# Optimization experiments

Hardware: AMD Instinct MI355X
Metric: run time of the kernel (lower is better)

The kernel has to match this reference:

```python
import jax
import jax.numpy as jnp
from jax import lax
import numpy as np

D_MODEL = 768
D_INNER = 1536  # d_model * expand_factor
D_STATE = 16
D_CONV = 4
BATCH = 2
SEQ = 2048
EPS = 1e-5


def silu(x):
    return x * jax.nn.sigmoid(x)


def setup_inputs() -> dict:
    key = jax.random.key(0)
    ks = jax.random.split(key, 24)
    n = lambda k, shape, s=0.1: jax.random.normal(k, shape, dtype=jnp.float32) * s
    inp = {
        "x": jax.random.normal(ks[0], (BATCH, SEQ, D_MODEL), dtype=jnp.float32),
        "ln_g": jnp.ones((D_MODEL,), jnp.float32),
        "ln_b": jnp.zeros((D_MODEL,), jnp.float32),
        "W_in": n(ks[1], (D_INNER, D_MODEL)),
        "b_in": n(ks[2], (D_INNER,)),
        "conv_w": n(ks[3], (D_INNER, 1, D_CONV), 0.02),
        "conv_b": jnp.zeros((D_INNER,), jnp.float32),
        "W_A": n(ks[4], (D_STATE, D_INNER)),
        "b_A": n(ks[5], (D_STATE,)),
        "W_B": n(ks[6], (D_STATE, D_INNER)),
        "b_B": n(ks[7], (D_STATE,)),
        "W_C": n(ks[8], (D_STATE, D_INNER)),
        "b_C": n(ks[9], (D_STATE,)),
        "W_dt": n(ks[10], (D_STATE, D_INNER)),
        "b_dt": n(ks[11], (D_STATE,)),
        "W_S": n(ks[12], (2 * D_INNER, D_INNER)),
        "b_S": n(ks[13], (2 * D_INNER,)),
        "W_gate": n(ks[14], (D_INNER, D_MODEL)),
        "b_gate": n(ks[15], (D_INNER,)),
        "W_out": n(ks[16], (D_MODEL, D_INNER)),
        "b_out": n(ks[17], (D_MODEL,)),
    }
    return inp


def reference(x, ln_g, ln_b, W_in, b_in, conv_w, conv_b, W_A, b_A, W_B, b_B,
              W_C, b_C, W_dt, b_dt, W_S, b_S, W_gate, b_gate, W_out, b_out):
    residual = x
    # LayerNorm
    mu = jnp.mean(x, axis=-1, keepdims=True)
    var = jnp.mean((x - mu) ** 2, axis=-1, keepdims=True)
    xn = (x - mu) * lax.rsqrt(var + EPS) * ln_g + ln_b
    # in projection -> [B, S, D_INNER]
    xp = xn @ W_in.T + b_in
    # depthwise causal conv1d over time
    k = conv_w.shape[-1]
    xc = jnp.moveaxis(xp, 1, 2)  # [B, D, L]
    xc = lax.conv_general_dilated(
        xc, conv_w, window_strides=(1,), padding=[(k - 1, 0)],
        dimension_numbers=("NCH", "OIH", "NCH"),
        feature_group_count=xc.shape[1])
    xc = xc + conv_b[None, :, None]
    xa = silu(jnp.moveaxis(xc, 1, 2))  # [B, S, D]
    # selective gating of SSM input (S_b computed but unused, as in source)
    S = xa @ W_S.T + b_S
    d = xa.shape[-1]
    S_a = jax.nn.sigmoid(S[..., :d])
    u = xa * S_a  # [B, S, D]
    # input-dependent SSM params [B, S, N]
    A = -jnp.exp(u @ W_A.T + b_A)
    dt = jnp.exp(u @ W_dt.T + b_dt)
    Bm = u @ W_B.T + b_B
    Cm = u @ W_C.T + b_C
    decay = jnp.exp(A * dt)  # [B, S, N]

    def step(h, inputs):
        dec_t, B_t, C_t, u_t = inputs  # [B,N],[B,N],[B,N],[B,D]
        h = h * dec_t[:, None, :] + B_t[:, None, :] * u_t[:, :, None]  # [B,D,N]
        y = jnp.einsum("bdn,bn->bd", h, C_t)
        return h, y

    h0 = jnp.zeros((u.shape[0], u.shape[2], decay.shape[-1]), u.dtype)
    scan_in = (jnp.moveaxis(decay, 1, 0), jnp.moveaxis(Bm, 1, 0),
               jnp.moveaxis(Cm, 1, 0), jnp.moveaxis(u, 1, 0))
    _, ys = lax.scan(step, h0, scan_in)
    y = jnp.moveaxis(ys, 0, 1)  # [B, S, D]
    # output gating + projection + residual
    gate = silu(xn @ W_gate.T + b_gate)
    out = (gate * y) @ W_out.T + b_out + residual
    return out
```

## Files before the change

### kernel.cpp

```cpp
#include <hip/hip_runtime.h>


typedef unsigned short u16;
using short8 = __attribute__((ext_vector_type(8))) short;
using f32x4  = __attribute__((ext_vector_type(4))) float;

#define BATCH 2
#define SEQ   2048
#define DM    768
#define DI    1536
#define NIG   (2*DI)
#define NST   16
#define LCH   64
#define NCH   32
#define NTOK  (BATCH*SEQ)

__device__ __forceinline__ u16 f2b(float x) {
  unsigned u = __float_as_uint(x);
  u += 0x7FFFu + ((u >> 16) & 1u);
  return (u16)(u >> 16);
}
__device__ __forceinline__ float b2f(u16 v) { return __uint_as_float((unsigned)v << 16); }
__device__ __forceinline__ float sigmoidf_(float x) { return 1.f / (1.f + expf(-x)); }
__device__ __forceinline__ float siluf_(float x) { return x / (1.f + expf(-x)); }

#define N_IG   (NIG * DM / 4)
#define N_WS   (DI * DI / 4)
#define N_WO   (DM * DI / 4)
#define N_WAB  (64 * DI / 4)
#define N_CAST (N_IG + N_WS + N_WO + N_WAB + NIG + 64)

__global__ __launch_bounds__(256) void cast_all(
    const float* __restrict__ Wi, const float* __restrict__ Wg,
    const float* __restrict__ bi, const float* __restrict__ bg,
    const float* __restrict__ WS, const float* __restrict__ WO,
    const float* __restrict__ WA, const float* __restrict__ Wdt,
    const float* __restrict__ WB, const float* __restrict__ WC,
    const float* __restrict__ bA, const float* __restrict__ bdt,
    const float* __restrict__ bB, const float* __restrict__ bC,
    u16* __restrict__ Wigb, float* __restrict__ biasig,
    u16* __restrict__ WSb, u16* __restrict__ Woutb,
    u16* __restrict__ Wabcd, float* __restrict__ bias64) {
  int i = blockIdx.x * 256 + threadIdx.x;
  if (i < N_IG) {
    int i4 = i * 4, r = i4 / DM, c = i4 % DM;
    const float* src = (r < DI) ? Wi + (size_t)r * DM + c : Wg + (size_t)(r - DI) * DM + c;
    float4 v = *(const float4*)src;
    ushort4 o; o.x = f2b(v.x); o.y = f2b(v.y); o.z = f2b(v.z); o.w = f2b(v.w);
    ((ushort4*)Wigb)[i] = o;
  } else if (i < N_IG + N_WS) {
    int j = i - N_IG;
    float4 v = ((const float4*)WS)[j];
    ushort4 o; o.x = f2b(v.x); o.y = f2b(v.y); o.z = f2b(v.z); o.w = f2b(v.w);
    ((ushort4*)WSb)[j] = o;
  } else if (i < N_IG + N_WS + N_WO) {
    int j = i - N_IG - N_WS;
    float4 v = ((const float4*)WO)[j];
    ushort4 o; o.x = f2b(v.x); o.y = f2b(v.y); o.z = f2b(v.z); o.w = f2b(v.w);
    ((ushort4*)Woutb)[j] = o;
  } else if (i < N_IG + N_WS + N_WO + N_WAB) {
    int j = i - N_IG - N_WS - N_WO;
    int i4 = j * 4, r = i4 / DI, c = i4 % DI;
    const float* src = (r < 16) ? WA + (size_t)r * DI
                     : (r < 32) ? Wdt + (size_t)(r - 16) * DI
                     : (r < 48) ? WB + (size_t)(r - 32) * DI
                                : WC + (size_t)(r - 48) * DI;
    float4 v = *(const float4*)(src + c);
    ushort4 o; o.x = f2b(v.x); o.y = f2b(v.y); o.z = f2b(v.z); o.w = f2b(v.w);
    ((ushort4*)Wabcd)[j] = o;
  } else if (i < N_IG + N_WS + N_WO + N_WAB + NIG) {
    int j = i - N_IG - N_WS - N_WO - N_WAB;
    biasig[j] = (j < DI) ? bi[j] : bg[j - DI];
  } else if (i < N_CAST) {
    int j = i - N_IG - N_WS - N_WO - N_WAB - NIG;
    bias64[j] = (j < 16) ? bA[j] : (j < 32) ? bdt[j - 16] : (j < 48) ? bB[j - 32] : bC[j - 48];
  }
}

__global__ __launch_bounds__(256) void ln_kernel(const float* __restrict__ x, const float* __restrict__ g,
                                                 const float* __restrict__ bb, u16* __restrict__ xn) {
  int m = blockIdx.x, tid = threadIdx.x;
  const float* xr = x + (size_t)m * DM;
  float v0 = xr[tid], v1 = xr[tid + 256], v2 = xr[tid + 512];
  float s  = v0 + v1 + v2;
  float s2 = fmaf(v0, v0, fmaf(v1, v1, v2 * v2));
  #pragma unroll
  for (int off = 32; off > 0; off >>= 1) { s += __shfl_down(s, off); s2 += __shfl_down(s2, off); }
  __shared__ float sh[8];
  int wave = tid >> 6, lane = tid & 63;
  if (lane == 0) { sh[wave] = s; sh[4 + wave] = s2; }
  __syncthreads();
  float S1 = sh[0] + sh[1] + sh[2] + sh[3];
  float S2 = sh[4] + sh[5] + sh[6] + sh[7];
  float mu = S1 * (1.f / DM);
  float var = S2 * (1.f / DM) - mu * mu;
  float rs = rsqrtf(var + 1e-5f);
  u16* o = xn + (size_t)m * DM;
  o[tid]       = f2b((v0 - mu) * rs * g[tid]       + bb[tid]);
  o[tid + 256] = f2b((v1 - mu) * rs * g[tid + 256] + bb[tid + 256]);
  o[tid + 512] = f2b((v2 - mu) * rs * g[tid + 512] + bb[tid + 512]);
}

__device__ __forceinline__ void gll16(const void* g, void* l) {
  __builtin_amdgcn_global_load_lds((const __attribute__((address_space(1))) void*)g,
                                   (__attribute__((address_space(3))) void*)l, 16, 0, 0);
}

template <int MODE, int BM>
__global__ __launch_bounds__(BM == 128 ? 512 : 256) void gemm_bt(
    const u16* __restrict__ A, const u16* __restrict__ B,
    const float* __restrict__ bias, const float* __restrict__ aux,
    const u16* __restrict__ auxb,
    float* __restrict__ C, u16* __restrict__ Cb,
    int M, int N, int K) {
  __shared__ __align__(16) u16 As[3][BM * 32];
  __shared__ __align__(16) u16 Bs[3][128 * 32];
  const int tid = threadIdx.x, wave = tid >> 6, lane = tid & 63;

  const int nbx = gridDim.x, nwg = nbx * gridDim.y;
  const int orig = blockIdx.y * nbx + blockIdx.x;
  const int cpx = nwg >> 3;
  const int swz = (orig & 7) * cpx + (orig >> 3);
  const int m0 = (swz / nbx) * BM, n0 = (swz % nbx) * 128;

  const int wm = (wave >> 1) * 32, wn = (wave & 1) * 64;
  const int fr = lane & 15, fq = lane >> 4;
  f32x4 acc[2][4] = {};

  const int c0 = tid;
  const u16* Ag0 = A + (size_t)(m0 + (c0 >> 2)) * K + ((c0 & 3) ^ ((c0 >> 3) & 3)) * 8;
  const u16* Bg0 = B + (size_t)(n0 + (c0 >> 2)) * K + ((c0 & 3) ^ ((c0 >> 3) & 3)) * 8;
  const int lofs = (wave * 64) * 8;
  const int c1 = tid + 256;
  const u16* Bg1 = B + (size_t)(n0 + (c1 >> 2)) * K + ((c1 & 3) ^ ((c1 >> 3) & 3)) * 8;
  const int lofs1 = (256 + wave * 64) * 8;

  int offA[2], offB[4];
  #pragma unroll
  for (int i = 0; i < 2; ++i) {
    int ra = wm + i * 16 + fr;
    offA[i] = ra * 32 + (fq ^ ((ra >> 1) & 3)) * 8;
  }
  #pragma unroll
  for (int i = 0; i < 4; ++i) {
    int rb = wn + i * 16 + fr;
    offB[i] = rb * 32 + (fq ^ ((rb >> 1) & 3)) * 8;
  }

  const int nk = K >> 5;

#define STAGE_BT(tt) { const int bb_ = (tt) % 3; \
                       gll16(Ag0 + (tt) * 32, (u16*)As[bb_] + lofs); \
                       gll16(Bg0 + (tt) * 32, (u16*)Bs[bb_] + lofs); \
                       if (BM == 64) gll16(Bg1 + (tt) * 32, (u16*)Bs[bb_] + lofs1); }
#define COMPUTE_BT(tt) { const u16* as_ = As[(tt) % 3]; const u16* bs_ = Bs[(tt) % 3]; \
    short8 av[2], bv[4]; \
    _Pragma("unroll") for (int i = 0; i < 2; ++i) av[i] = *(const short8*)(as_ + offA[i]); \
    _Pragma("unroll") for (int i = 0; i < 4; ++i) bv[i] = *(const short8*)(bs_ + offB[i]); \
    __builtin_amdgcn_s_setprio(1); \
    _Pragma("unroll") for (int mi = 0; mi < 2; ++mi) \
      _Pragma("unroll") for (int ni = 0; ni < 4; ++ni) \
        acc[mi][ni] = __builtin_amdgcn_mfma_f32_16x16x32_bf16(av[mi], bv[ni], acc[mi][ni], 0, 0, 0); \
    __builtin_amdgcn_s_setprio(0); }
#define WAIT1S() { if (BM == 128) asm volatile("s_waitcnt vmcnt(2)" ::: "memory"); \
                   else           asm volatile("s_waitcnt vmcnt(3)" ::: "memory"); }

  STAGE_BT(0); STAGE_BT(1);

  for (int t = 0; t < nk - 2; ++t) {
    WAIT1S();
    __builtin_amdgcn_s_barrier();
    STAGE_BT(t + 2);
    COMPUTE_BT(t);
  }
  WAIT1S();
  __builtin_amdgcn_s_barrier();
  COMPUTE_BT(nk - 2);
  asm volatile("s_waitcnt vmcnt(0)" ::: "memory");
  __builtin_amdgcn_s_barrier();
  COMPUTE_BT(nk - 1);
#undef STAGE_BT
#undef COMPUTE_BT
#undef WAIT1S

  #pragma unroll
  for (int ni = 0; ni < 4; ++ni) {
    int col = n0 + wn + ni * 16 + fr;
    float bv_ = bias[col];
    #pragma unroll
    for (int mi = 0; mi < 2; ++mi) {
      int row = m0 + wm + mi * 16 + fq * 4;
      #pragma unroll
      for (int j = 0; j < 4; ++j) {
        size_t off = (size_t)(row + j) * N + col;
        float z = acc[mi][ni][j] + bv_;
        if (MODE == 0) {
          C[off] = z + aux[off];
        } else if (MODE == 1) {
          Cb[off] = f2b(b2f(auxb[off]) * sigmoidf_(z));
        } else {
          Cb[off] = f2b(z);
        }
      }
    }
  }
}

__global__ __launch_bounds__(256) void gemm_abcd(const u16* __restrict__ A, const u16* __restrict__ B,
                                                 float* __restrict__ Zp, int M, int K) {
  __shared__ __align__(16) u16 As[2][64 * 64];
  __shared__ __align__(16) u16 Bs[2][64 * 64];
  const int tid = threadIdx.x, wave = tid >> 6, lane = tid & 63;
  const int m0 = blockIdx.x * 64;
  const int ks = blockIdx.y;
  const int Kq = K >> 2;
  const int kbase = ks * Kq;
  const int wm = wave * 16;
  const int fr = lane & 15, fq = lane >> 4;
  f32x4 acc[4] = {};

  const int c0 = tid, c1 = tid + 256;
  const u16* Ag0 = A + (size_t)(m0 + (c0 >> 3)) * K + kbase + ((c0 & 7) ^ ((c0 >> 3) & 7)) * 8;
  const u16* Ag1 = A + (size_t)(m0 + (c1 >> 3)) * K + kbase + ((c1 & 7) ^ ((c1 >> 3) & 7)) * 8;
  const u16* Bg0 = B + (size_t)(c0 >> 3) * K + kbase + ((c0 & 7) ^ ((c0 >> 3) & 7)) * 8;
  const u16* Bg1 = B + (size_t)(c1 >> 3) * K + kbase + ((c1 & 7) ^ ((c1 >> 3) & 7)) * 8;
  const int lo0 = (wave * 64) * 8;
  const int lo1 = (256 + wave * 64) * 8;

  int offAv[2], offBv[2][4];
  {
    int r = wm + fr;
    #pragma unroll
    for (int kk = 0; kk < 2; ++kk) offAv[kk] = r * 64 + ((kk * 4 + fq) ^ (r & 7)) * 8;
    #pragma unroll
    for (int i = 0; i < 4; ++i) {
      int rb = i * 16 + fr;
      #pragma unroll
      for (int kk = 0; kk < 2; ++kk) offBv[kk][i] = rb * 64 + ((kk * 4 + fq) ^ (rb & 7)) * 8;
    }
  }

  const int nk = Kq >> 6;
  gll16(Ag0, (u16*)As[0] + lo0);
  gll16(Ag1, (u16*)As[0] + lo1);
  gll16(Bg0, (u16*)Bs[0] + lo0);
  gll16(Bg1, (u16*)Bs[0] + lo1);

  for (int t = 0; t < nk; ++t) {
    __syncthreads();
    if (t + 1 < nk) {
      int ko = (t + 1) * 64;
      gll16(Ag0 + ko, (u16*)As[(t + 1) & 1] + lo0);
      gll16(Ag1 + ko, (u16*)As[(t + 1) & 1] + lo1);
      gll16(Bg0 + ko, (u16*)Bs[(t + 1) & 1] + lo0);
      gll16(Bg1 + ko, (u16*)Bs[(t + 1) & 1] + lo1);
    }
    const u16* as = As[t & 1];
    const u16* bs = Bs[t & 1];
    #pragma unroll
    for (int kk = 0; kk < 2; ++kk) {
      short8 av = *(const short8*)(as + offAv[kk]);
      short8 bv[4];
      #pragma unroll
      for (int i = 0; i < 4; ++i) bv[i] = *(const short8*)(bs + offBv[kk][i]);
      #pragma unroll
      for (int ni = 0; ni < 4; ++ni)
        acc[ni] = __builtin_amdgcn_mfma_f32_16x16x32_bf16(av, bv[ni], acc[ni], 0, 0, 0);
    }
  }

  float* zp = Zp + (size_t)ks * M * 64;
  #pragma unroll
  for (int ni = 0; ni < 4; ++ni) {
    int col = ni * 16 + fr;
    #pragma unroll
    for (int j = 0; j < 4; ++j) {
      int row = m0 + wm + fq * 4 + j;
      zp[(size_t)row * 64 + col] = acc[ni][j];
    }
  }
}

__global__ __launch_bounds__(256) void abcd_combine(const float* __restrict__ Zp, const float* __restrict__ bias64,
                                                    float* __restrict__ dec, float* __restrict__ Bm,
                                                    float* __restrict__ Cm, int M) {
  int idx = blockIdx.x * 256 + threadIdx.x;
  int row = idx >> 4, n = idx & 15;
  float zA = bias64[n], zDt = bias64[16 + n], zB = bias64[32 + n], zC = bias64[48 + n];
  #pragma unroll
  for (int ks = 0; ks < 4; ++ks) {
    const float* zp = Zp + ((size_t)ks * M + row) * 64;
    zA += zp[n]; zDt += zp[16 + n]; zB += zp[32 + n]; zC += zp[48 + n];
  }
  size_t o = (size_t)row * NST + n;
  dec[o] = expf(-expf(zA + zDt));
  Bm[o] = zB;
  Cm[o] = zC;
}

__global__ __launch_bounds__(256) void conv_silu(const u16* __restrict__ xpg, const float* __restrict__ cw,
                                                 const float* __restrict__ cb, u16* __restrict__ xab) {
  int idx = blockIdx.x * 256 + threadIdx.x;
  int d8 = idx % (DI / 8);
  int token = idx / (DI / 8);
  int t = token % SEQ;
  int d0 = d8 * 8;
  const short8* xv = (const short8*)(xpg + (size_t)token * NIG + d0);
  short8 z8 = {0, 0, 0, 0, 0, 0, 0, 0};
  short8 x3 = (t >= 3) ? xv[-3 * (NIG / 8)] : z8;
  short8 x2 = (t >= 2) ? xv[-2 * (NIG / 8)] : z8;
  short8 x1 = (t >= 1) ? xv[-1 * (NIG / 8)] : z8;
  short8 x0 = xv[0];
  const float4* cw4 = (const float4*)cw;
  float4 cbl = ((const float4*)cb)[d8 * 2], cbh = ((const float4*)cb)[d8 * 2 + 1];
  float cbv[8] = {cbl.x, cbl.y, cbl.z, cbl.w, cbh.x, cbh.y, cbh.z, cbh.w};
  short8 o;
  #pragma unroll
  for (int j = 0; j < 8; ++j) {
    float4 w = cw4[d0 + j];
    float a = cbv[j];
    a = fmaf(b2f((u16)x3[j]), w.x, a);
    a = fmaf(b2f((u16)x2[j]), w.y, a);
    a = fmaf(b2f((u16)x1[j]), w.z, a);
    a = fmaf(b2f((u16)x0[j]), w.w, a);
    o[j] = (short)f2b(siluf_(a));
  }
  *(short8*)(xab + (size_t)token * DI + d0) = o;
}

__global__ __launch_bounds__(256) void scan_phase1(const u16* __restrict__ ub, const float* __restrict__ dec,
                                                   const float* __restrict__ Bm, u16* __restrict__ lend,
                                                   float* __restrict__ P) {
  __shared__ __align__(16) float dl[LCH * NST], bl[LCH * NST];
  int bid = blockIdx.x;
  int dblk = bid % 6, b = (bid / 6) % BATCH, c = bid / (6 * BATCH);
  int d = dblk * 256 + threadIdx.x;
  int t0 = c * LCH;
  size_t base16 = (size_t)(b * SEQ + t0) * NST;
  for (int i = threadIdx.x; i < LCH * NST / 4; i += 256) {
    ((float4*)dl)[i] = ((const float4*)(dec + base16))[i];
    ((float4*)bl)[i] = ((const float4*)(Bm + base16))[i];
  }
  __syncthreads();
  float h[NST];
  #pragma unroll
  for (int n = 0; n < NST; ++n) h[n] = 0.f;
  const u16* up = ub + (size_t)(b * SEQ + t0) * DI + d;
  for (int t = 0; t < LCH; ++t) {
    float uu = b2f(up[(size_t)t * DI]);
    const f32x4* d4 = (const f32x4*)(dl + t * NST);
    const f32x4* b4 = (const f32x4*)(bl + t * NST);
    #pragma unroll
    for (int q = 0; q < 4; ++q) {
      f32x4 dd = d4[q], bb = b4[q];
      #pragma unroll
      for (int j = 0; j < 4; ++j) h[q * 4 + j] = fmaf(h[q * 4 + j], dd[j], bb[j] * uu);
    }
  }
  u16* lo = lend + ((size_t)(c * BATCH + b) * DI + d) * NST;
  short8 s0, s1;
  #pragma unroll
  for (int n = 0; n < 8; ++n) { s0[n] = (short)f2b(h[n]); s1[n] = (short)f2b(h[8 + n]); }
  ((short8*)lo)[0] = s0;
  ((short8*)lo)[1] = s1;
  if (dblk == 0 && threadIdx.x < NST) {
    float pr = 1.f;
    for (int t = 0; t < LCH; ++t) pr *= dl[t * NST + threadIdx.x];
    P[(size_t)(c * BATCH + b) * NST + threadIdx.x] = pr;
  }
}

__global__ __launch_bounds__(256) void scan_phase2(const u16* __restrict__ lend, const float* __restrict__ P,
                                                   u16* __restrict__ Hin) {
  int flat = blockIdx.x * 256 + threadIdx.x;
  int n = flat & 15;
  int d = (flat >> 4) % DI;
  int b = flat / (DI * NST);
  float h = 0.f;
  for (int c = 0; c < NCH; ++c) {
    size_t idx = ((size_t)(c * BATCH + b) * DI + d) * NST + n;
    Hin[idx] = f2b(h);
    h = fmaf(P[(size_t)(c * BATCH + b) * NST + n], h, b2f(lend[idx]));
  }
}

__global__ __launch_bounds__(256) void scan_phase3(const u16* __restrict__ ub, const float* __restrict__ dec,
                                                   const float* __restrict__ Bm, const float* __restrict__ Cm,
                                                   const u16* __restrict__ Hin, const u16* __restrict__ xpg,
                                                   u16* __restrict__ gy) {
  __shared__ __align__(16) float dl[LCH * NST], bl[LCH * NST], cl[LCH * NST];
  int bid = blockIdx.x;
  int dblk = bid % 6, b = (bid / 6) % BATCH, c = bid / (6 * BATCH);
  int d = dblk * 256 + threadIdx.x;
  int t0 = c * LCH;
  size_t base16 = (size_t)(b * SEQ + t0) * NST;
  for (int i = threadIdx.x; i < LCH * NST / 4; i += 256) {
    ((float4*)dl)[i] = ((const float4*)(dec + base16))[i];
    ((float4*)bl)[i] = ((const float4*)(Bm + base16))[i];
    ((float4*)cl)[i] = ((const float4*)(Cm + base16))[i];
  }
  __syncthreads();
  float h[NST];
  const short8* hi = (const short8*)(Hin + ((size_t)(c * BATCH + b) * DI + d) * NST);
  short8 h0 = hi[0], h1 = hi[1];
  #pragma unroll
  for (int n = 0; n < 8; ++n) { h[n] = b2f((u16)h0[n]); h[8 + n] = b2f((u16)h1[n]); }
  const u16* up = ub + (size_t)(b * SEQ + t0) * DI + d;
  const u16* gp = xpg + (size_t)(b * SEQ + t0) * NIG + DI + d;
  u16* yp = gy + (size_t)(b * SEQ + t0) * DI + d;
  for (int t = 0; t < LCH; ++t) {
    float uu = b2f(up[(size_t)t * DI]);
    const f32x4* d4 = (const f32x4*)(dl + t * NST);
    const f32x4* b4 = (const f32x4*)(bl + t * NST);
    const f32x4* c4 = (const f32x4*)(cl + t * NST);
    float acc = 0.f;
    #pragma unroll
    for (int q = 0; q < 4; ++q) {
      f32x4 dd = d4[q], bb = b4[q], cc = c4[q];
      #pragma unroll
      for (int j = 0; j < 4; ++j) {
        h[q * 4 + j] = fmaf(h[q * 4 + j], dd[j], bb[j] * uu);
        acc = fmaf(h[q * 4 + j], cc[j], acc);
      }
    }
    float g = b2f(gp[(size_t)t * NIG]);
    yp[(size_t)t * DI] = f2b(siluf_(g) * acc);
  }
}

extern "C" void kernel_launch(void* const* d_in, const int* in_sizes, int n_in,
                              void* d_out, int out_size, void* d_ws, size_t ws_size,
                              hipStream_t stream) {
  const float* x      = (const float*)d_in[0];
  const float* ln_g   = (const float*)d_in[1];
  const float* ln_b   = (const float*)d_in[2];
  const float* W_in   = (const float*)d_in[3];
  const float* b_in   = (const float*)d_in[4];
  const float* conv_w = (const float*)d_in[5];
  const float* conv_b = (const float*)d_in[6];
  const float* W_A    = (const float*)d_in[7];
  const float* b_A    = (const float*)d_in[8];
  const float* W_B    = (const float*)d_in[9];
  const float* b_B    = (const float*)d_in[10];
  const float* W_C    = (const float*)d_in[11];
  const float* b_C    = (const float*)d_in[12];
  const float* W_dt   = (const float*)d_in[13];
  const float* b_dt   = (const float*)d_in[14];
  const float* W_S    = (const float*)d_in[15];
  const float* b_S    = (const float*)d_in[16];
  const float* W_gate = (const float*)d_in[17];
  const float* b_gate = (const float*)d_in[18];
  const float* W_out  = (const float*)d_in[19];
  const float* b_out  = (const float*)d_in[20];
  float* out = (float*)d_out;

  char* p = (char*)d_ws;
  auto alloc = [&](size_t bytes) { char* r = p; p += (bytes + 255) & ~(size_t)255; return r; };
  u16*   Wigb    = (u16*)alloc((size_t)NIG * DM * 2);
  float* biasig  = (float*)alloc((size_t)NIG * 4);
  u16*   WSb     = (u16*)alloc((size_t)DI * DI * 2);
  u16*   Woutb   = (u16*)alloc((size_t)DM * DI * 2);
  u16*   Wabcd   = (u16*)alloc((size_t)64 * DI * 2);
  float* bias64  = (float*)alloc(64 * 4);
  u16*   xnb     = (u16*)alloc((size_t)NTOK * DM * 2);
  u16*   xpg     = (u16*)alloc((size_t)NTOK * NIG * 2);
  u16*   xab     = (u16*)alloc((size_t)NTOK * DI * 2);
  u16*   ub      = (u16*)alloc((size_t)NTOK * DI * 2);
  float* Zp      = (float*)alloc((size_t)4 * NTOK * 64 * 4);
  float* decb    = (float*)alloc((size_t)NTOK * NST * 4);
  float* Bmb     = (float*)alloc((size_t)NTOK * NST * 4);
  float* Cmb     = (float*)alloc((size_t)NTOK * NST * 4);
  u16*   lend    = (u16*)alloc((size_t)NCH * BATCH * DI * NST * 2);
  u16*   Hin     = (u16*)alloc((size_t)NCH * BATCH * DI * NST * 2);
  float* P       = (float*)alloc((size_t)NCH * BATCH * NST * 4);
  u16* gy = xab;

  cast_all<<<(N_CAST + 255) / 256, 256, 0, stream>>>(W_in, W_gate, b_in, b_gate, W_S, W_out,
                                                     W_A, W_dt, W_B, W_C, b_A, b_dt, b_B, b_C,
                                                     Wigb, biasig, WSb, Woutb, Wabcd, bias64);

  ln_kernel<<<NTOK, 256, 0, stream>>>(x, ln_g, ln_b, xnb);

  gemm_bt<2, 128><<<dim3(NIG / 128, NTOK / 128), 512, 0, stream>>>(xnb, Wigb, biasig, nullptr, nullptr,
                                                                   nullptr, xpg, NTOK, NIG, DM);

  conv_silu<<<NTOK * (DI / 8) / 256, 256, 0, stream>>>(xpg, conv_w, conv_b, xab);

  gemm_bt<1, 128><<<dim3(DI / 128, NTOK / 128), 512, 0, stream>>>(xab, WSb, b_S, nullptr, xab,
                                                                  nullptr, ub, NTOK, DI, DI);

  gemm_abcd<<<dim3(NTOK / 64, 4), 256, 0, stream>>>(ub, Wabcd, Zp, NTOK, DI);
  abcd_combine<<<NTOK * 16 / 256, 256, 0, stream>>>(Zp, bias64, decb, Bmb, Cmb, NTOK);

  scan_phase1<<<NCH * BATCH * (DI / 256), 256, 0, stream>>>(ub, decb, Bmb, lend, P);
  scan_phase2<<<BATCH * DI * NST / 256, 256, 0, stream>>>(lend, P, Hin);
  scan_phase3<<<NCH * BATCH * (DI / 256), 256, 0, stream>>>(ub, decb, Bmb, Cmb, Hin, xpg, gy);

  gemm_bt<0, 64><<<dim3(DM / 128, NTOK / 64), 256, 0, stream>>>(gy, Woutb, b_out, x, nullptr,
                                                                out, nullptr, NTOK, DM, DI);
}
```

Before: 195.2 us.

## Add 32x32x16 MFMA GEMM kernel for input and gating projections

```diff
diff --git a/kernel.cpp b/kernel.cpp
--- a/kernel.cpp
+++ b/kernel.cpp
@@ -4,6 +4,7 @@
 typedef unsigned short u16;
 using short8 = __attribute__((ext_vector_type(8))) short;
 using f32x4  = __attribute__((ext_vector_type(4))) float;
+using f32x16 = __attribute__((ext_vector_type(16))) float;
 
 #define BATCH 2
 #define SEQ   2048
@@ -106,6 +107,104 @@
                                    (__attribute__((address_space(3))) void*)l, 16, 0, 0);
 }
 
+template <int MODE>
+__global__ __launch_bounds__(256) void gemm32(
+    const u16* __restrict__ A, const u16* __restrict__ B,
+    const float* __restrict__ bias, const u16* __restrict__ auxb,
+    u16* __restrict__ Cb, int M, int N, int K) {
+  __shared__ __align__(16) u16 As[3][128 * 32];
+  __shared__ __align__(16) u16 Bs[3][128 * 32];
+  const int tid = threadIdx.x, wave = tid >> 6, lane = tid & 63;
+
+  const int nbx = gridDim.x, nwg = nbx * gridDim.y;
+  const int orig = blockIdx.y * nbx + blockIdx.x;
+  const int cpx = nwg >> 3;
+  const int swz = (orig & 7) * cpx + (orig >> 3);
+  const int m0 = (swz / nbx) * 128, n0 = (swz % nbx) * 128;
+
+  const int wm = (wave >> 1) * 64, wn = (wave & 1) * 64;
+  const int lr = lane & 31, lh = lane >> 5;
+  f32x16 acc[2][2] = {};
+
+  const int c0 = tid, c1 = tid + 256;
+  const u16* Ag0 = A + (size_t)(m0 + (c0 >> 2)) * K + ((c0 & 3) ^ ((c0 >> 3) & 3)) * 8;
+  const u16* Ag1 = A + (size_t)(m0 + (c1 >> 2)) * K + ((c1 & 3) ^ ((c1 >> 3) & 3)) * 8;
+  const u16* Bg0 = B + (size_t)(n0 + (c0 >> 2)) * K + ((c0 & 3) ^ ((c0 >> 3) & 3)) * 8;
+  const u16* Bg1 = B + (size_t)(n0 + (c1 >> 2)) * K + ((c1 & 3) ^ ((c1 >> 3) & 3)) * 8;
+  const int lo0 = (wave * 64) * 8;
+  const int lo1 = (256 + wave * 64) * 8;
+
+  int offA[2][2], offB[2][2];
+  #pragma unroll
+  for (int mi = 0; mi < 2; ++mi)
+    #pragma unroll
+    for (int kk = 0; kk < 2; ++kk) {
+      int ra = wm + mi * 32 + lr;
+      int rb = wn + mi * 32 + lr;
+      int q = kk * 2 + lh;
+      offA[mi][kk] = ra * 32 + ((q ^ ((ra >> 1) & 3))) * 8;
+      offB[mi][kk] = rb * 32 + ((q ^ ((rb >> 1) & 3))) * 8;
+    }
+
+  const int nk = K >> 5;
+
+#define STAGE32(tt) { const int bb_ = (tt) % 3; \
+    gll16(Ag0 + (tt) * 32, (u16*)As[bb_] + lo0); \
+    gll16(Ag1 + (tt) * 32, (u16*)As[bb_] + lo1); \
+    gll16(Bg0 + (tt) * 32, (u16*)Bs[bb_] + lo0); \
+    gll16(Bg1 + (tt) * 32, (u16*)Bs[bb_] + lo1); }
+#define COMPUTE32(tt) { const u16* as_ = As[(tt) % 3]; const u16* bs_ = Bs[(tt) % 3]; \
+    short8 av[2][2], bv[2][2]; \
+    _Pragma("unroll") for (int mi = 0; mi < 2; ++mi) \
+      _Pragma("unroll") for (int kk = 0; kk < 2; ++kk) { \
+        av[mi][kk] = *(const short8*)(as_ + offA[mi][kk]); \
+        bv[mi][kk] = *(const short8*)(bs_ + offB[mi][kk]); } \
+    __builtin_amdgcn_s_setprio(1); \
+    _Pragma("unroll") for (int kk = 0; kk < 2; ++kk) \
+      _Pragma("unroll") for (int mi = 0; mi < 2; ++mi) \
+        _Pragma("unroll") for (int ni = 0; ni < 2; ++ni) \
+          acc[mi][ni] = __builtin_amdgcn_mfma_f32_32x32x16_bf16(av[mi][kk], bv[ni][kk], acc[mi][ni], 0, 0, 0); \
+    __builtin_amdgcn_s_setprio(0); }
+
+  STAGE32(0); STAGE32(1);
+
+  for (int t = 0; t < nk - 2; ++t) {
+    asm volatile("s_waitcnt vmcnt(4)" ::: "memory");
+    __builtin_amdgcn_s_barrier();
+    STAGE32(t + 2);
+    COMPUTE32(t);
+  }
+  asm volatile("s_waitcnt vmcnt(4)" ::: "memory");
+  __builtin_amdgcn_s_barrier();
+  COMPUTE32(nk - 2);
+  asm volatile("s_waitcnt vmcnt(0)" ::: "memory");
+  __builtin_amdgcn_s_barrier();
+  COMPUTE32(nk - 1);
+#undef STAGE32
+#undef COMPUTE32
+
+  #pragma unroll
+  for (int ni = 0; ni < 2; ++ni) {
+    int col = n0 + wn + ni * 32 + lr;
+    float bv_ = bias[col];
+    #pragma unroll
+    for (int mi = 0; mi < 2; ++mi) {
+      int rbase = m0 + wm + mi * 32 + 4 * lh;
+      #pragma unroll
+      for (int reg = 0; reg < 16; ++reg) {
+        int row = rbase + (reg & 3) + 8 * (reg >> 2);
+        size_t off = (size_t)row * N + col;
+        float z = acc[mi][ni][reg] + bv_;
+        if (MODE == 1) {
+          Cb[off] = f2b(b2f(auxb[off]) * sigmoidf_(z));
+        } else {
+          Cb[off] = f2b(z);
+        }
+      }
+    }
+  }
+}
+
 template <int MODE, int BM>
 __global__ __launch_bounds__(BM == 128 ? 512 : 256) void gemm_bt(
     const u16* __restrict__ A, const u16* __restrict__ B,
@@ -481,13 +580,13 @@
 
   ln_kernel<<<NTOK, 256, 0, stream>>>(x, ln_g, ln_b, xnb);
 
-  gemm_bt<2, 128><<<dim3(NIG / 128, NTOK / 128), 512, 0, stream>>>(xnb, Wigb, biasig, nullptr, nullptr,
-                                                                   nullptr, xpg, NTOK, NIG, DM);
+  gemm32<2><<<dim3(NIG / 128, NTOK / 128), 256, 0, stream>>>(xnb, Wigb, biasig, nullptr,
+                                                             xpg, NTOK, NIG, DM);
 
   conv_silu<<<NTOK * (DI / 8) / 256, 256, 0, stream>>>(xpg, conv_w, conv_b, xab);
 
-  gemm_bt<1, 128><<<dim3(DI / 128, NTOK / 128), 512, 0, stream>>>(xab, WSb, b_S, nullptr, xab,
-                                                                  nullptr, ub, NTOK, DI, DI);
+  gemm32<1><<<dim3(DI / 128, NTOK / 128), 256, 0, stream>>>(xab, WSb, b_S, xab,
+                                                            ub, NTOK, DI, DI);
 
   gemm_abcd<<<dim3(NTOK / 64, 4), 256, 0, stream>>>(ub, Wabcd, Zp, NTOK, DI);
   abcd_combine<<<NTOK * 16 / 256, 256, 0, stream>>>(Zp, bias64, decb, Bmb, Cmb, NTOK);
```

Measured after the change: 202.7 us. 3.9% more time.

## Double K-tile depth to 64 with double-buffered LDS pipeline in GEMM

Applied to the files above, without the earlier changes.

```diff
diff --git a/kernel.cpp b/kernel.cpp
--- a/kernel.cpp
+++ b/kernel.cpp
@@ -113,9 +113,10 @@
     const u16* __restrict__ auxb,
     float* __restrict__ C, u16* __restrict__ Cb,
     int M, int N, int K) {
-  __shared__ __align__(16) u16 As[3][BM * 32];
-  __shared__ __align__(16) u16 Bs[3][128 * 32];
+  __shared__ __align__(16) u16 As[2][BM * 64];
+  __shared__ __align__(16) u16 Bs[2][128 * 64];
   const int tid = threadIdx.x, wave = tid >> 6, lane = tid & 63;
+  const int NT = (BM == 128 ? 512 : 256);
 
   const int nbx = gridDim.x, nwg = nbx * gridDim.y;
   const int orig = blockIdx.y * nbx + blockIdx.x;
@@ -127,61 +128,58 @@
   const int fr = lane & 15, fq = lane >> 4;
   f32x4 acc[2][4] = {};
 
-  const int c0 = tid;
-  const u16* Ag0 = A + (size_t)(m0 + (c0 >> 2)) * K + ((c0 & 3) ^ ((c0 >> 3) & 3)) * 8;
-  const u16* Bg0 = B + (size_t)(n0 + (c0 >> 2)) * K + ((c0 & 3) ^ ((c0 >> 3) & 3)) * 8;
-  const int lofs = (wave * 64) * 8;
-  const int c1 = tid + 256;
-  const u16* Bg1 = B + (size_t)(n0 + (c1 >> 2)) * K + ((c1 & 3) ^ ((c1 >> 3) & 3)) * 8;
-  const int lofs1 = (256 + wave * 64) * 8;
-
-  int offA[2], offB[4];
-  #pragma unroll
-  for (int i = 0; i < 2; ++i) {
-    int ra = wm + i * 16 + fr;
-    offA[i] = ra * 32 + (fq ^ ((ra >> 1) & 3)) * 8;
-  }
-  #pragma unroll
-  for (int i = 0; i < 4; ++i) {
-    int rb = wn + i * 16 + fr;
-    offB[i] = rb * 32 + (fq ^ ((rb >> 1) & 3)) * 8;
-  }
-
-  const int nk = K >> 5;
-
-#define STAGE_BT(tt) { const int bb_ = (tt) % 3; \
-                       gll16(Ag0 + (tt) * 32, (u16*)As[bb_] + lofs); \
-                       gll16(Bg0 + (tt) * 32, (u16*)Bs[bb_] + lofs); \
-                       if (BM == 64) gll16(Bg1 + (tt) * 32, (u16*)Bs[bb_] + lofs1); }
-#define COMPUTE_BT(tt) { const u16* as_ = As[(tt) % 3]; const u16* bs_ = Bs[(tt) % 3]; \
-    short8 av[2], bv[4]; \
-    _Pragma("unroll") for (int i = 0; i < 2; ++i) av[i] = *(const short8*)(as_ + offA[i]); \
-    _Pragma("unroll") for (int i = 0; i < 4; ++i) bv[i] = *(const short8*)(bs_ + offB[i]); \
-    __builtin_amdgcn_s_setprio(1); \
-    _Pragma("unroll") for (int mi = 0; mi < 2; ++mi) \
-      _Pragma("unroll") for (int ni = 0; ni < 4; ++ni) \
-        acc[mi][ni] = __builtin_amdgcn_mfma_f32_16x16x32_bf16(av[mi], bv[ni], acc[mi][ni], 0, 0, 0); \
-    __builtin_amdgcn_s_setprio(0); }
-#define WAIT1S() { if (BM == 128) asm volatile("s_waitcnt vmcnt(2)" ::: "memory"); \
-                   else           asm volatile("s_waitcnt vmcnt(3)" ::: "memory"); }
-
-  STAGE_BT(0); STAGE_BT(1);
-
-  for (int t = 0; t < nk - 2; ++t) {
-    WAIT1S();
+  const int srow = tid >> 3;
+  const u16* Ag0 = A + (size_t)(m0 + srow) * K + (((tid & 7) ^ (srow & 7))) * 8;
+  const u16* Bg0 = B + (size_t)(n0 + srow) * K + (((tid & 7) ^ (srow & 7))) * 8;
+  const int rstep = NT >> 3;
+  const int lbase = (wave * 64) * 8;
+  const int lstep = NT * 8;
+
+  int offA[2][2], offB[2][4];
+  #pragma unroll
+  for (int kk = 0; kk < 2; ++kk) {
+    #pragma unroll
+    for (int i = 0; i < 2; ++i) {
+      int ra = wm + i * 16 + fr;
+      offA[kk][i] = ra * 64 + (((kk * 4 + fq) ^ (ra & 7))) * 8;
+    }
+    #pragma unroll
+    for (int i = 0; i < 4; ++i) {
+      int rb = wn + i * 16 + fr;
+      offB[kk][i] = rb * 64 + (((kk * 4 + fq) ^ (rb & 7))) * 8;
+    }
+  }
+
+  const int nk = K >> 6;
+
+#define STAGE_BT(tt) { const int bb_ = (tt) & 1; const int ko_ = (tt) * 64; \
+    gll16(Ag0 + ko_,                     (u16*)As[bb_] + lbase); \
+    gll16(Ag0 + (size_t)rstep * K + ko_, (u16*)As[bb_] + lstep + lbase); \
+    gll16(Bg0 + ko_,                     (u16*)Bs[bb_] + lbase); \
+    gll16(Bg0 + (size_t)rstep * K + ko_, (u16*)Bs[bb_] + lstep + lbase); \
+    if (BM == 64) { \
+      gll16(Bg0 + (size_t)2 * rstep * K + ko_, (u16*)Bs[bb_] + 2 * lstep + lbase); \
+      gll16(Bg0 + (size_t)3 * rstep * K + ko_, (u16*)Bs[bb_] + 3 * lstep + lbase); } }
+#define COMPUTE_BT(tt) { const u16* as_ = As[(tt) & 1]; const u16* bs_ = Bs[(tt) & 1]; \
+    _Pragma("unroll") for (int kk = 0; kk < 2; ++kk) { \
+      short8 av[2], bv[4]; \
+      _Pragma("unroll") for (int i = 0; i < 2; ++i) av[i] = *(const short8*)(as_ + offA[kk][i]); \
+      _Pragma("unroll") for (int i = 0; i < 4; ++i) bv[i] = *(const short8*)(bs_ + offB[kk][i]); \
+      __builtin_amdgcn_s_setprio(1); \
+      _Pragma("unroll") for (int mi = 0; mi < 2; ++mi) \
+        _Pragma("unroll") for (int ni = 0; ni < 4; ++ni) \
+          acc[mi][ni] = __builtin_amdgcn_mfma_f32_16x16x32_bf16(av[mi], bv[ni], acc[mi][ni], 0, 0, 0); \
+      __builtin_amdgcn_s_setprio(0); } }
+
+  STAGE_BT(0);
+  for (int t = 0; t < nk; ++t) {
+    asm volatile("s_waitcnt vmcnt(0)" ::: "memory");
     __builtin_amdgcn_s_barrier();
-    STAGE_BT(t + 2);
+    if (t + 1 < nk) STAGE_BT(t + 1);
     COMPUTE_BT(t);
   }
-  WAIT1S();
-  __builtin_amdgcn_s_barrier();
-  COMPUTE_BT(nk - 2);
-  asm volatile("s_waitcnt vmcnt(0)" ::: "memory");
-  __builtin_amdgcn_s_barrier();
-  COMPUTE_BT(nk - 1);
 #undef STAGE_BT
 #undef COMPUTE_BT
-#undef WAIT1S
 
   #pragma unroll
   for (int ni = 0; ni < 4; ++ni) {
```

Measured after the change: 184.9 us. -5.3%, faster.
